# Kernel tuning notes

Hardware: AMD Instinct MI355X
Metric: run time of the kernel (lower is better)

The kernel has to match this reference:

```python
import jax, jax.numpy as jnp
import numpy as np

H, W = 200, 200           # BEV spatial shape (single level)
NBQ, NH, NL, NP = 2, 8, 1, 4
D = 256
HD = D // NH


def setup_inputs() -> dict:
    key = jax.random.key(0)
    ks = jax.random.split(key, 12)
    bs, nq = 1, H * W
    query = jax.random.normal(ks[0], (bs, nq, D), jnp.float32)
    value = jax.random.normal(ks[1], (bs, NBQ * nq, D), jnp.float32)
    reference_points = jax.random.uniform(ks[2], (bs, nq, NL, 2), dtype=jnp.float32)
    spatial_shapes = jnp.array([[H, W]], dtype=jnp.int32)
    sc = 1.0 / np.sqrt(D)
    W_v = jax.random.normal(ks[3], (D, D), jnp.float32) * sc
    b_v = jax.random.normal(ks[4], (D,), jnp.float32) * 0.01
    W_so = jax.random.normal(ks[5], (2 * D, NBQ * NH * NL * NP * 2), jnp.float32) * 0.02
    b_so = jax.random.normal(ks[6], (NBQ * NH * NL * NP * 2,), jnp.float32) * 0.5
    W_aw = jax.random.normal(ks[7], (2 * D, NBQ * NH * NL * NP), jnp.float32) * 0.02
    b_aw = jax.random.normal(ks[8], (NBQ * NH * NL * NP,), jnp.float32) * 0.01
    W_o = jax.random.normal(ks[9], (D, D), jnp.float32) * sc
    b_o = jax.random.normal(ks[10], (D,), jnp.float32) * 0.01
    return {"query": query, "value": value, "reference_points": reference_points,
            "spatial_shapes": spatial_shapes,
            "W_v": W_v, "b_v": b_v, "W_so": W_so, "b_so": b_so,
            "W_aw": W_aw, "b_aw": b_aw, "W_o": W_o, "b_o": b_o}


def _ms_deform_attn(value, locs, attn):
    # value: (B, K, NH, HD); locs: (B, nq, NH, NL, NP, 2) in [0,1]; attn: (B, nq, NH, NL, NP)
    B, K, h, d = value.shape
    nq = locs.shape[1]
    out = jnp.zeros((B, nq, h, d), value.dtype)
    start = 0
    for l, (Hl, Wl) in enumerate([(H, W)]):
        v = value[:, start:start + Hl * Wl].transpose(0, 2, 1, 3).reshape(B * h, Hl * Wl, d)
        start += Hl * Wl
        g = locs[:, :, :, l]                      # (B, nq, h, NP, 2)
        # grid_sample(align_corners=False, padding='zeros') pixel coords
        x = g[..., 0] * Wl - 0.5
        y = g[..., 1] * Hl - 0.5
        x0 = jnp.floor(x); y0 = jnp.floor(y)
        lx = x - x0; ly = y - y0
        x0 = x0.astype(jnp.int32); y0 = y0.astype(jnp.int32)
        acc = jnp.zeros((B * h, nq * NP, d), value.dtype)
        for dy, wy in ((0, 1.0 - ly), (1, ly)):
            for dx, wx in ((0, 1.0 - lx), (1, lx)):
                xi = x0 + dx; yi = y0 + dy
                valid = ((xi >= 0) & (xi < Wl) & (yi >= 0) & (yi < Hl)).astype(value.dtype)
                idx = jnp.clip(yi, 0, Hl - 1) * Wl + jnp.clip(xi, 0, Wl - 1)  # (B,nq,h,NP)
                idxf = idx.transpose(0, 2, 1, 3).reshape(B * h, nq * NP)
                samp = jnp.take_along_axis(v, idxf[:, :, None], axis=1)       # (B*h, nq*NP, d)
                wgt = (wx * wy * valid).transpose(0, 2, 1, 3).reshape(B * h, nq * NP, 1)
                acc = acc + samp * wgt
        acc = acc.reshape(B, h, nq, NP, d)
        out = out + jnp.einsum('bhqpd,bqhp->bqhd', acc, attn[:, :, :, l])
    return out.reshape(B, nq, h * d)


def reference(query, value, reference_points, spatial_shapes,
              W_v, b_v, W_so, b_so, W_aw, b_aw, W_o, b_o):
    bs, nq, _ = query.shape
    identity = query
    val4 = value.reshape(bs, NBQ, nq, D)
    # query enhanced with most recent bev-queue features
    qe = jnp.concatenate([val4[:, 0], query], axis=-1)           # (bs, nq, 2D)
    vproj = (value @ W_v + b_v).reshape(bs * NBQ, nq, NH, HD)
    off = (qe @ W_so + b_so).reshape(bs, nq, NH, NBQ, NL, NP, 2)
    aw = (qe @ W_aw + b_aw).reshape(bs, nq, NH, NBQ, NL * NP)
    aw = jax.nn.softmax(aw, axis=-1).reshape(bs, nq, NH, NBQ, NL, NP)
    aw = aw.transpose(0, 3, 1, 2, 4, 5).reshape(bs * NBQ, nq, NH, NL, NP)
    # offset normalizer: [W, H] per level
    norm = jnp.stack([spatial_shapes[:, 1], spatial_shapes[:, 0]], -1).astype(query.dtype)  # (NL,2)
    locs = (reference_points[:, :, None, None, :, None, :]
            + off / norm[None, None, None, None, :, None, :])     # (bs,nq,NH,NBQ,NL,NP,2)
    locs = locs.transpose(0, 3, 1, 2, 4, 5, 6).reshape(bs * NBQ, nq, NH, NL, NP, 2)
    out = _ms_deform_attn(vproj, locs, aw)                        # (bs*NBQ, nq, D)
    out = out.reshape(bs, NBQ, nq, D).mean(axis=1)
    return out @ W_o + b_o + identity
```

## Files before the change

### kernel.cpp

```cpp
#include <hip/hip_runtime.h>
#include <math.h>

#define HW_   40000
#define NQ_   40000
#define IMGW  200
#define IMGH  200

typedef __bf16 bf16;
typedef __attribute__((ext_vector_type(4))) __bf16 bf16x4;
typedef __attribute__((ext_vector_type(8))) __bf16 bf16x8;
typedef __attribute__((ext_vector_type(4))) float f32x4;

__global__ __launch_bounds__(256) void cast_transpose_kernel(
    const float* __restrict__ B, bf16* __restrict__ Bt, int K, int N, int ldt)
{
  int idx = blockIdx.x * 256 + threadIdx.x;
  if (idx >= K * N) return;
  int k = idx / N, n = idx - k * N;
  Bt[(size_t)n * ldt + k] = (bf16)B[idx];
}

template<int KT, int MODE>
__global__ __launch_bounds__(256) void mfma_gemm_kernel(
    const float* __restrict__ A0, const float* __restrict__ A1,
    const bf16* __restrict__ Bt,
    const float* __restrict__ bias0, const float* __restrict__ bias1,
    const float* __restrict__ resid,
    void* __restrict__ outp, void* __restrict__ outp2,
    int M, int N)
{
  __shared__ bf16 As[128][40];
  __shared__ bf16 Bs[128][40];
  const int t    = threadIdx.x;
  const int m0   = blockIdx.y * 128;
  const int n0   = blockIdx.x * 128;
  const int w    = t >> 6;
  const int lane = t & 63;
  const int quad = lane >> 4;
  const int l16  = lane & 15;
  const int wm   = (w & 1) * 64;
  const int wn   = (w >> 1) * 64;

  f32x4 acc[4][4] = {};

  const int sa_row = t >> 3;
  const int sa_k   = (t & 7) * 4;
  const int sb_row = t >> 2;
  const int sb_k   = (t & 3) * 8;

  for (int kt = 0; kt < KT; kt += 32) {
    __syncthreads();
#pragma unroll
    for (int i = 0; i < 4; ++i) {
      int m  = i * 32 + sa_row;
      int gm = m0 + m; if (gm >= M) gm = M - 1;
      int gk = kt + sa_k;
      const float* Ap;
      int col;
      if (KT == 512) { Ap = (gk < 256) ? A0 : A1; col = gk & 255; }
      else           { Ap = A0; col = gk; }
      float4 av = *(const float4*)&Ap[(size_t)gm * 256 + col];
      bf16x4 bv = { (bf16)av.x, (bf16)av.y, (bf16)av.z, (bf16)av.w };
      *(bf16x4*)&As[m][sa_k] = bv;
    }
#pragma unroll
    for (int i = 0; i < 2; ++i) {
      int n  = i * 64 + sb_row;
      int gn = n0 + n; if (gn >= N) gn = N - 1;
      float4 bv = *(const float4*)&Bt[(size_t)gn * KT + kt + sb_k];
      *(float4*)&Bs[n][sb_k] = bv;
    }
    __syncthreads();
    bf16x8 af[4], bfr[4];
#pragma unroll
    for (int x = 0; x < 4; ++x) {
      af[x]  = *(const bf16x8*)&As[wm + x * 16 + l16][quad * 8];
      bfr[x] = *(const bf16x8*)&Bs[wn + x * 16 + l16][quad * 8];
    }
#pragma unroll
    for (int mt = 0; mt < 4; ++mt)
#pragma unroll
      for (int nt = 0; nt < 4; ++nt)
        acc[mt][nt] = __builtin_amdgcn_mfma_f32_16x16x32_bf16(
            af[mt], bfr[nt], acc[mt][nt], 0, 0, 0);
  }

#pragma unroll
  for (int mt = 0; mt < 4; ++mt) {
#pragma unroll
    for (int r = 0; r < 4; ++r) {
      const int gm = m0 + wm + mt * 16 + quad * 4 + r;
      if (gm >= M) continue;
#pragma unroll
      for (int nt = 0; nt < 4; ++nt) {
        const int gn = n0 + wn + nt * 16 + l16;
        float v = acc[mt][nt][r];
        if (MODE == 0) {
          int nbq = (gm >= HW_) ? 1 : 0;
          int pix = gm - nbq * HW_;
          int h = gn >> 5, hd = gn & 31;
          ((bf16*)outp)[(((size_t)(nbq * 8 + h) * HW_ + pix) << 5) + hd] =
              (bf16)(v + bias0[gn]);
        } else if (MODE == 1) {
          if (gn < 128)
            ((float*)outp)[(size_t)gm * 128 + gn] = v + bias0[gn];
          else if (gn < 192)
            ((float*)outp2)[(size_t)gm * 64 + (gn - 128)] = v + bias1[gn - 128];
        } else {
          ((float*)outp)[(size_t)gm * 256 + gn] =
              v + bias0[gn] + resid[(size_t)gm * 256 + gn];
        }
      }
    }
  }
}

__global__ __launch_bounds__(256) void deform_attn_kernel(
    const bf16*  __restrict__ vws,
    const float* __restrict__ off_ws,
    const float* __restrict__ aw_ws,
    const float* __restrict__ ref,
    float* __restrict__ ms)
{
  const int q  = blockIdx.x;
  const int t  = threadIdx.x;
  const int h  = t >> 5;
  const int hd = t & 31;
  const float rx = ref[2 * q + 0] * (float)IMGW - 0.5f;
  const float ry = ref[2 * q + 1] * (float)IMGH - 0.5f;
  float acc = 0.0f;
#pragma unroll
  for (int nbq = 0; nbq < 2; ++nbq) {
    const int g = h * 2 + nbq;
    const float4 a4 = *(const float4*)&aw_ws[(size_t)q * 64 + g * 4];
    float mx = fmaxf(fmaxf(a4.x, a4.y), fmaxf(a4.z, a4.w));
    float e0 = __expf(a4.x - mx), e1 = __expf(a4.y - mx);
    float e2 = __expf(a4.z - mx), e3 = __expf(a4.w - mx);
    float inv = 1.0f / (e0 + e1 + e2 + e3);
    float w4[4] = {e0 * inv, e1 * inv, e2 * inv, e3 * inv};
    const float4 o01 = *(const float4*)&off_ws[(size_t)q * 128 + g * 8];
    const float4 o23 = *(const float4*)&off_ws[(size_t)q * 128 + g * 8 + 4];
    float ox[4] = {o01.x, o01.z, o23.x, o23.z};
    float oy[4] = {o01.y, o01.w, o23.y, o23.w};
    const bf16* vbase = vws + (((size_t)(nbq * 8 + h) * HW_) << 5) + hd;
#pragma unroll
    for (int p = 0; p < 4; ++p) {
      float x = rx + ox[p];
      float y = ry + oy[p];
      float xf = floorf(x), yf = floorf(y);
      int   x0 = (int)xf,   y0 = (int)yf;
      float lx = x - xf,    ly = y - yf;
      int   x1 = x0 + 1,    y1 = y0 + 1;
      float w00 = (1.0f - lx) * (1.0f - ly);
      float w01 = lx * (1.0f - ly);
      float w10 = (1.0f - lx) * ly;
      float w11 = lx * ly;
      if (x0 < 0 || x0 >= IMGW) { w00 = 0.0f; w10 = 0.0f; }
      if (x1 < 0 || x1 >= IMGW) { w01 = 0.0f; w11 = 0.0f; }
      if (y0 < 0 || y0 >= IMGH) { w00 = 0.0f; w01 = 0.0f; }
      if (y1 < 0 || y1 >= IMGH) { w10 = 0.0f; w11 = 0.0f; }
      int xc0 = min(max(x0, 0), IMGW - 1), xc1 = min(max(x1, 0), IMGW - 1);
      int yc0 = min(max(y0, 0), IMGH - 1), yc1 = min(max(y1, 0), IMGH - 1);
      float v00 = (float)vbase[(size_t)(yc0 * IMGW + xc0) << 5];
      float v01 = (float)vbase[(size_t)(yc0 * IMGW + xc1) << 5];
      float v10 = (float)vbase[(size_t)(yc1 * IMGW + xc0) << 5];
      float v11 = (float)vbase[(size_t)(yc1 * IMGW + xc1) << 5];
      float s = w00 * v00 + w01 * v01 + w10 * v10 + w11 * v11;
      acc = fmaf(w4[p], s, acc);
    }
  }
  ms[(size_t)q * 256 + t] = 0.5f * acc;
}

extern "C" void kernel_launch(void* const* d_in, const int* in_sizes, int n_in,
                              void* d_out, int out_size, void* d_ws, size_t ws_size,
                              hipStream_t stream) {
  const float* query = (const float*)d_in[0];
  const float* value = (const float*)d_in[1];
  const float* ref   = (const float*)d_in[2];
  const float* Wv  = (const float*)d_in[4];
  const float* bv  = (const float*)d_in[5];
  const float* Wso = (const float*)d_in[6];
  const float* bso = (const float*)d_in[7];
  const float* Waw = (const float*)d_in[8];
  const float* baw = (const float*)d_in[9];
  const float* Wo  = (const float*)d_in[10];
  const float* bo  = (const float*)d_in[11];
  float* out = (float*)d_out;

  char* p = (char*)d_ws;
  bf16*  vws    = (bf16*)p;  p += (size_t)2 * 8 * HW_ * 32 * 2;
  float* off_ws = (float*)p; p += (size_t)NQ_ * 128 * 4;
  float* aw_ws  = (float*)p; p += (size_t)NQ_ * 64 * 4;
  float* ms     = (float*)p; p += (size_t)NQ_ * 256 * 4;
  bf16*  BtV    = (bf16*)p;  p += (size_t)256 * 256 * 2;
  bf16*  BtOA   = (bf16*)p;  p += (size_t)192 * 512 * 2;
  bf16*  BtO    = (bf16*)p;  p += (size_t)256 * 256 * 2;

  cast_transpose_kernel<<<(256 * 256 + 255) / 256, 256, 0, stream>>>(Wv, BtV, 256, 256, 256);
  cast_transpose_kernel<<<(512 * 128 + 255) / 256, 256, 0, stream>>>(Wso, BtOA, 512, 128, 512);
  cast_transpose_kernel<<<(512 * 64 + 255) / 256, 256, 0, stream>>>(Waw, BtOA + (size_t)128 * 512, 512, 64, 512);
  cast_transpose_kernel<<<(256 * 256 + 255) / 256, 256, 0, stream>>>(Wo, BtO, 256, 256, 256);

  mfma_gemm_kernel<256, 0><<<dim3(2, 625), 256, 0, stream>>>(
      value, nullptr, BtV, bv, nullptr, nullptr, vws, nullptr, 2 * HW_, 256);
  mfma_gemm_kernel<512, 1><<<dim3(2, 313), 256, 0, stream>>>(
      value, query, BtOA, bso, baw, nullptr, off_ws, aw_ws, NQ_, 192);
  deform_attn_kernel<<<dim3(NQ_), 256, 0, stream>>>(vws, off_ws, aw_ws, ref, ms);
  mfma_gemm_kernel<256, 2><<<dim3(2, 313), 256, 0, stream>>>(
      ms, nullptr, BtO, bo, nullptr, query, out, nullptr, NQ_, 256);
}
```

Measured before the change: 364.7 us.

## Pre-cast activations to bf16, use direct global-to-LDS loads, vectorize deform gather

Activations are cast to bf16 in separate pre-pass kernels, so the GEMMs load bf16 tiles straight into LDS with global_load_lds instead of converting fp32 in registers. Offsets, attention logits and the sampled-output intermediate are now stored as bf16, which halves their traffic. The deformable sampling kernel is rebuilt so each lane gathers 8 channels with vector loads, 4 queries run per block, and the two queue frames are summed with a lane shuffle. The cost is extra cast passes over value and query, bf16 rounding of sampling offsets (a position-accuracy risk), and an LDS layout without padding that may cause bank conflicts.

```diff
diff --git a/kernel.cpp b/kernel.cpp
--- a/kernel.cpp
+++ b/kernel.cpp
@@ -11,6 +11,24 @@
 typedef __attribute__((ext_vector_type(8))) __bf16 bf16x8;
 typedef __attribute__((ext_vector_type(4))) float f32x4;
 
+__device__ __forceinline__ void gload_lds16(const void* g, void* l) {
+  __builtin_amdgcn_global_load_lds(
+      (const __attribute__((address_space(1))) void*)g,
+      (__attribute__((address_space(3))) void*)l, 16, 0, 0);
+}
+
+__global__ __launch_bounds__(256) void cast_f32_bf16_kernel(
+    const float* __restrict__ src, bf16* __restrict__ dst, int n8)
+{
+  int i = blockIdx.x * 256 + threadIdx.x;
+  if (i >= n8) return;
+  const float4 a = ((const float4*)src)[2 * i];
+  const float4 b = ((const float4*)src)[2 * i + 1];
+  bf16x8 o = {(bf16)a.x, (bf16)a.y, (bf16)a.z, (bf16)a.w,
+              (bf16)b.x, (bf16)b.y, (bf16)b.z, (bf16)b.w};
+  *(bf16x8*)&dst[(size_t)i * 8] = o;
+}
+
 __global__ __launch_bounds__(256) void cast_transpose_kernel(
     const float* __restrict__ B, bf16* __restrict__ Bt, int K, int N, int ldt)
 {
@@ -22,15 +40,15 @@
 
 template<int KT, int MODE>
 __global__ __launch_bounds__(256) void mfma_gemm_kernel(
-    const float* __restrict__ A0, const float* __restrict__ A1,
+    const bf16* __restrict__ A0, const bf16* __restrict__ A1,
     const bf16* __restrict__ Bt,
     const float* __restrict__ bias0, const float* __restrict__ bias1,
     const float* __restrict__ resid,
     void* __restrict__ outp, void* __restrict__ outp2,
     int M, int N)
 {
-  __shared__ bf16 As[128][40];
-  __shared__ bf16 Bs[128][40];
+  __shared__ bf16 As[128 * 32];
+  __shared__ bf16 Bs[128 * 32];
   const int t    = threadIdx.x;
   const int m0   = blockIdx.y * 128;
   const int n0   = blockIdx.x * 128;
@@ -43,39 +61,35 @@
 
   f32x4 acc[4][4] = {};
 
-  const int sa_row = t >> 3;
-  const int sa_k   = (t & 7) * 4;
-  const int sb_row = t >> 2;
-  const int sb_k   = (t & 3) * 8;
+  const int srow  = t >> 2;
+  const int skoff = (t & 3) * 8;
+  bf16* ldsA0 = As + t * 8;
+  bf16* ldsA1 = As + 2048 + t * 8;
+  bf16* ldsB0 = Bs + t * 8;
+  bf16* ldsB1 = Bs + 2048 + t * 8;
+
+  int gmA0 = m0 + srow;      if (gmA0 >= M) gmA0 = M - 1;
+  int gmA1 = m0 + 64 + srow; if (gmA1 >= M) gmA1 = M - 1;
+  int gnB0 = n0 + srow;      if (gnB0 >= N) gnB0 = N - 1;
+  int gnB1 = n0 + 64 + srow; if (gnB1 >= N) gnB1 = N - 1;
 
   for (int kt = 0; kt < KT; kt += 32) {
+    const bf16* Ap;
+    int col;
+    if (KT == 512) { Ap = (kt < 256) ? A0 : A1; col = kt & 255; }
+    else           { Ap = A0; col = kt; }
     __syncthreads();
-#pragma unroll
-    for (int i = 0; i < 4; ++i) {
-      int m  = i * 32 + sa_row;
-      int gm = m0 + m; if (gm >= M) gm = M - 1;
-      int gk = kt + sa_k;
-      const float* Ap;
-      int col;
-      if (KT == 512) { Ap = (gk < 256) ? A0 : A1; col = gk & 255; }
-      else           { Ap = A0; col = gk; }
-      float4 av = *(const float4*)&Ap[(size_t)gm * 256 + col];
-      bf16x4 bv = { (bf16)av.x, (bf16)av.y, (bf16)av.z, (bf16)av.w };
-      *(bf16x4*)&As[m][sa_k] = bv;
-    }
-#pragma unroll
-    for (int i = 0; i < 2; ++i) {
-      int n  = i * 64 + sb_row;
-      int gn = n0 + n; if (gn >= N) gn = N - 1;
-      float4 bv = *(const float4*)&Bt[(size_t)gn * KT + kt + sb_k];
-      *(float4*)&Bs[n][sb_k] = bv;
-    }
+    gload_lds16(&Ap[(size_t)gmA0 * 256 + col + skoff], ldsA0);
+    gload_lds16(&Ap[(size_t)gmA1 * 256 + col + skoff], ldsA1);
+    gload_lds16(&Bt[(size_t)gnB0 * KT + kt + skoff], ldsB0);
+    gload_lds16(&Bt[(size_t)gnB1 * KT + kt + skoff], ldsB1);
     __syncthreads();
+
     bf16x8 af[4], bfr[4];
 #pragma unroll
     for (int x = 0; x < 4; ++x) {
-      af[x]  = *(const bf16x8*)&As[wm + x * 16 + l16][quad * 8];
-      bfr[x] = *(const bf16x8*)&Bs[wn + x * 16 + l16][quad * 8];
+      af[x]  = *(const bf16x8*)&As[(wm + x * 16 + l16) * 32 + quad * 8];
+      bfr[x] = *(const bf16x8*)&Bs[(wn + x * 16 + l16) * 32 + quad * 8];
     }
 #pragma unroll
     for (int mt = 0; mt < 4; ++mt)
@@ -103,9 +117,10 @@
               (bf16)(v + bias0[gn]);
         } else if (MODE == 1) {
           if (gn < 128)
-            ((float*)outp)[(size_t)gm * 128 + gn] = v + bias0[gn];
+            ((bf16*)outp)[(size_t)gm * 128 + gn] = (bf16)(v + bias0[gn]);
           else if (gn < 192)
-            ((float*)outp2)[(size_t)gm * 64 + (gn - 128)] = v + bias1[gn - 128];
+            ((bf16*)outp2)[(size_t)gm * 64 + (gn - 128)] =
+                (bf16)(v + bias1[gn - 128]);
         } else {
           ((float*)outp)[(size_t)gm * 256 + gn] =
               v + bias0[gn] + resid[(size_t)gm * 256 + gn];
@@ -116,60 +131,79 @@
 }
 
 __global__ __launch_bounds__(256) void deform_attn_kernel(
-    const bf16*  __restrict__ vws,
-    const float* __restrict__ off_ws,
-    const float* __restrict__ aw_ws,
+    const bf16* __restrict__ vws,
+    const bf16* __restrict__ off_bf,
+    const bf16* __restrict__ aw_bf,
     const float* __restrict__ ref,
-    float* __restrict__ ms)
-{
-  const int q  = blockIdx.x;
-  const int t  = threadIdx.x;
-  const int h  = t >> 5;
-  const int hd = t & 31;
+    bf16* __restrict__ ms)
+{
+  const int t    = threadIdx.x;
+  const int w    = t >> 6;
+  const int lane = t & 63;
+  const int q    = blockIdx.x * 4 + w;
+  const int g    = lane >> 2;
+  const int sub  = lane & 3;
+  const int h    = g >> 1;
+  const int nbq  = g & 1;
+
   const float rx = ref[2 * q + 0] * (float)IMGW - 0.5f;
   const float ry = ref[2 * q + 1] * (float)IMGH - 0.5f;
-  float acc = 0.0f;
-#pragma unroll
-  for (int nbq = 0; nbq < 2; ++nbq) {
-    const int g = h * 2 + nbq;
-    const float4 a4 = *(const float4*)&aw_ws[(size_t)q * 64 + g * 4];
-    float mx = fmaxf(fmaxf(a4.x, a4.y), fmaxf(a4.z, a4.w));
-    float e0 = __expf(a4.x - mx), e1 = __expf(a4.y - mx);
-    float e2 = __expf(a4.z - mx), e3 = __expf(a4.w - mx);
-    float inv = 1.0f / (e0 + e1 + e2 + e3);
-    float w4[4] = {e0 * inv, e1 * inv, e2 * inv, e3 * inv};
-    const float4 o01 = *(const float4*)&off_ws[(size_t)q * 128 + g * 8];
-    const float4 o23 = *(const float4*)&off_ws[(size_t)q * 128 + g * 8 + 4];
-    float ox[4] = {o01.x, o01.z, o23.x, o23.z};
-    float oy[4] = {o01.y, o01.w, o23.y, o23.w};
-    const bf16* vbase = vws + (((size_t)(nbq * 8 + h) * HW_) << 5) + hd;
-#pragma unroll
-    for (int p = 0; p < 4; ++p) {
-      float x = rx + ox[p];
-      float y = ry + oy[p];
-      float xf = floorf(x), yf = floorf(y);
-      int   x0 = (int)xf,   y0 = (int)yf;
-      float lx = x - xf,    ly = y - yf;
-      int   x1 = x0 + 1,    y1 = y0 + 1;
-      float w00 = (1.0f - lx) * (1.0f - ly);
-      float w01 = lx * (1.0f - ly);
-      float w10 = (1.0f - lx) * ly;
-      float w11 = lx * ly;
-      if (x0 < 0 || x0 >= IMGW) { w00 = 0.0f; w10 = 0.0f; }
-      if (x1 < 0 || x1 >= IMGW) { w01 = 0.0f; w11 = 0.0f; }
-      if (y0 < 0 || y0 >= IMGH) { w00 = 0.0f; w01 = 0.0f; }
-      if (y1 < 0 || y1 >= IMGH) { w10 = 0.0f; w11 = 0.0f; }
-      int xc0 = min(max(x0, 0), IMGW - 1), xc1 = min(max(x1, 0), IMGW - 1);
-      int yc0 = min(max(y0, 0), IMGH - 1), yc1 = min(max(y1, 0), IMGH - 1);
-      float v00 = (float)vbase[(size_t)(yc0 * IMGW + xc0) << 5];
-      float v01 = (float)vbase[(size_t)(yc0 * IMGW + xc1) << 5];
-      float v10 = (float)vbase[(size_t)(yc1 * IMGW + xc0) << 5];
-      float v11 = (float)vbase[(size_t)(yc1 * IMGW + xc1) << 5];
-      float s = w00 * v00 + w01 * v01 + w10 * v10 + w11 * v11;
-      acc = fmaf(w4[p], s, acc);
+
+  bf16x4 a4 = *(const bf16x4*)&aw_bf[(size_t)q * 64 + g * 4];
+  float aa0 = (float)a4[0], aa1 = (float)a4[1], aa2 = (float)a4[2], aa3 = (float)a4[3];
+  float mx = fmaxf(fmaxf(aa0, aa1), fmaxf(aa2, aa3));
+  float e0 = __expf(aa0 - mx), e1 = __expf(aa1 - mx);
+  float e2 = __expf(aa2 - mx), e3 = __expf(aa3 - mx);
+  float inv = 1.0f / (e0 + e1 + e2 + e3);
+  float w4[4] = {e0 * inv, e1 * inv, e2 * inv, e3 * inv};
+
+  bf16x8 o8 = *(const bf16x8*)&off_bf[(size_t)q * 128 + g * 8];
+  float ox[4] = {(float)o8[0], (float)o8[2], (float)o8[4], (float)o8[6]};
+  float oy[4] = {(float)o8[1], (float)o8[3], (float)o8[5], (float)o8[7]};
+
+  const bf16* vbase = vws + (((size_t)(nbq * 8 + h) * HW_) << 5) + sub * 8;
+
+  float acc[8] = {};
+#pragma unroll
+  for (int p = 0; p < 4; ++p) {
+    float x = rx + ox[p];
+    float y = ry + oy[p];
+    float xf = floorf(x), yf = floorf(y);
+    int   x0 = (int)xf,   y0 = (int)yf;
+    float lx = x - xf,    ly = y - yf;
+    int   x1 = x0 + 1,    y1 = y0 + 1;
+    float w00 = (1.0f - lx) * (1.0f - ly);
+    float w01 = lx * (1.0f - ly);
+    float w10 = (1.0f - lx) * ly;
+    float w11 = lx * ly;
+    if (x0 < 0 || x0 >= IMGW) { w00 = 0.0f; w10 = 0.0f; }
+    if (x1 < 0 || x1 >= IMGW) { w01 = 0.0f; w11 = 0.0f; }
+    if (y0 < 0 || y0 >= IMGH) { w00 = 0.0f; w01 = 0.0f; }
+    if (y1 < 0 || y1 >= IMGH) { w10 = 0.0f; w11 = 0.0f; }
+    int xc0 = min(max(x0, 0), IMGW - 1), xc1 = min(max(x1, 0), IMGW - 1);
+    int yc0 = min(max(y0, 0), IMGH - 1), yc1 = min(max(y1, 0), IMGH - 1);
+    bf16x8 v00 = *(const bf16x8*)&vbase[(size_t)(yc0 * IMGW + xc0) << 5];
+    bf16x8 v01 = *(const bf16x8*)&vbase[(size_t)(yc0 * IMGW + xc1) << 5];
+    bf16x8 v10 = *(const bf16x8*)&vbase[(size_t)(yc1 * IMGW + xc0) << 5];
+    bf16x8 v11 = *(const bf16x8*)&vbase[(size_t)(yc1 * IMGW + xc1) << 5];
+    float wp = w4[p];
+#pragma unroll
+    for (int j = 0; j < 8; ++j) {
+      float s = w00 * (float)v00[j] + w01 * (float)v01[j] +
+                w10 * (float)v10[j] + w11 * (float)v11[j];
+      acc[j] = fmaf(wp, s, acc[j]);
     }
   }
-  ms[(size_t)q * 256 + t] = 0.5f * acc;
+
+#pragma unroll
+  for (int j = 0; j < 8; ++j) acc[j] += __shfl_xor(acc[j], 4);
+
+  if (nbq == 0) {
+    bf16x8 o;
+#pragma unroll
+    for (int j = 0; j < 8; ++j) o[j] = (bf16)(0.5f * acc[j]);
+    *(bf16x8*)&ms[(size_t)q * 256 + h * 32 + sub * 8] = o;
+  }
 }
 
 extern "C" void kernel_launch(void* const* d_in, const int* in_sizes, int n_in,
@@ -189,24 +223,28 @@
   float* out = (float*)d_out;
 
   char* p = (char*)d_ws;
-  bf16*  vws    = (bf16*)p;  p += (size_t)2 * 8 * HW_ * 32 * 2;
-  float* off_ws = (float*)p; p += (size_t)NQ_ * 128 * 4;
-  float* aw_ws  = (float*)p; p += (size_t)NQ_ * 64 * 4;
-  float* ms     = (float*)p; p += (size_t)NQ_ * 256 * 4;
-  bf16*  BtV    = (bf16*)p;  p += (size_t)256 * 256 * 2;
-  bf16*  BtOA   = (bf16*)p;  p += (size_t)192 * 512 * 2;
-  bf16*  BtO    = (bf16*)p;  p += (size_t)256 * 256 * 2;
-
-  cast_transpose_kernel<<<(256 * 256 + 255) / 256, 256, 0, stream>>>(Wv, BtV, 256, 256, 256);
-  cast_transpose_kernel<<<(512 * 128 + 255) / 256, 256, 0, stream>>>(Wso, BtOA, 512, 128, 512);
-  cast_transpose_kernel<<<(512 * 64 + 255) / 256, 256, 0, stream>>>(Waw, BtOA + (size_t)128 * 512, 512, 64, 512);
-  cast_transpose_kernel<<<(256 * 256 + 255) / 256, 256, 0, stream>>>(Wo, BtO, 256, 256, 256);
+  bf16* vws    = (bf16*)p; p += (size_t)2 * 8 * HW_ * 32 * 2;
+  bf16* off_bf = (bf16*)p; p += (size_t)NQ_ * 128 * 2;
+  bf16* aw_bf  = (bf16*)p; p += (size_t)NQ_ * 64 * 2;
+  bf16* ms     = (bf16*)p; p += (size_t)NQ_ * 256 * 2;
+  bf16* vbf    = (bf16*)p; p += (size_t)2 * HW_ * 256 * 2;
+  bf16* qbf    = (bf16*)p; p += (size_t)NQ_ * 256 * 2;
+  bf16* BtV    = (bf16*)p; p += (size_t)256 * 256 * 2;
+  bf16* BtOA   = (bf16*)p; p += (size_t)192 * 512 * 2;
+  bf16* BtO    = (bf16*)p; p += (size_t)256 * 256 * 2;
+
+  cast_f32_bf16_kernel<<<10000, 256, 0, stream>>>(value, vbf, 2 * HW_ * 256 / 8);
+  cast_f32_bf16_kernel<<<5000, 256, 0, stream>>>(query, qbf, NQ_ * 256 / 8);
+  cast_transpose_kernel<<<256, 256, 0, stream>>>(Wv, BtV, 256, 256, 256);
+  cast_transpose_kernel<<<256, 256, 0, stream>>>(Wso, BtOA, 512, 128, 512);
+  cast_transpose_kernel<<<128, 256, 0, stream>>>(Waw, BtOA + (size_t)128 * 512, 512, 64, 512);
+  cast_transpose_kernel<<<256, 256, 0, stream>>>(Wo, BtO, 256, 256, 256);
 
   mfma_gemm_kernel<256, 0><<<dim3(2, 625), 256, 0, stream>>>(
-      value, nullptr, BtV, bv, nullptr, nullptr, vws, nullptr, 2 * HW_, 256);
+      vbf, nullptr, BtV, bv, nullptr, nullptr, vws, nullptr, 2 * HW_, 256);
   mfma_gemm_kernel<512, 1><<<dim3(2, 313), 256, 0, stream>>>(
-      value, query, BtOA, bso, baw, nullptr, off_ws, aw_ws, NQ_, 192);
-  deform_attn_kernel<<<dim3(NQ_), 256, 0, stream>>>(vws, off_ws, aw_ws, ref, ms);
+      vbf, qbf, BtOA, bso, baw, nullptr, off_bf, aw_bf, NQ_, 192);
+  deform_attn_kernel<<<10000, 256, 0, stream>>>(vws, off_bf, aw_bf, ref, ms);
   mfma_gemm_kernel<256, 2><<<dim3(2, 313), 256, 0, stream>>>(
       ms, nullptr, BtO, bo, nullptr, query, out, nullptr, NQ_, 256);
 }
```

Result: faster. 340.1 us (-6.8%).
